# Performance work log

Hardware: AMD Instinct MI355X
Metric: run time of the kernel (lower is better)

Reference implementation:

```python
import jax, jax.numpy as jnp
import numpy as np

B, C, H, W = 32, 256, 32, 32   # batch, channels (inplanes==planes), spatial
E = 8                          # num_experts
EPS = 1e-5                     # BatchNorm eps


def setup_inputs() -> dict:
    key = jax.random.key(0)
    ks = jax.random.split(key, 6)
    s = 0.05
    return {
        "x": jax.random.normal(ks[0], (B, C, H, W), dtype=jnp.float32),
        # router: GAP -> Linear(C, E) -> sigmoid
        "router_w": jax.random.normal(ks[1], (E, C), dtype=jnp.float32) * s,
        "router_b": jnp.zeros((E,), dtype=jnp.float32),
        # expert kernel banks for the two CondConv2d layers (OIHW per expert)
        "w1": jax.random.normal(ks[2], (E, C, C, 3, 3), dtype=jnp.float32) * s,
        "w2": jax.random.normal(ks[3], (E, C, C, 3, 3), dtype=jnp.float32) * s,
        # BatchNorm (eval mode: running stats) params for bn1/bn2
        "g1": jnp.ones((C,), jnp.float32), "b1": jnp.zeros((C,), jnp.float32),
        "m1": jnp.zeros((C,), jnp.float32), "v1": jnp.ones((C,), jnp.float32),
        "g2": jnp.ones((C,), jnp.float32), "b2": jnp.zeros((C,), jnp.float32),
        "m2": jnp.zeros((C,), jnp.float32), "v2": jnp.ones((C,), jnp.float32),
    }


def _bn(x, g, b, m, v):
    # eval-mode BatchNorm over channel dim 1
    scale = (g * jax.lax.rsqrt(v + EPS))[None, :, None, None]
    shift = (b - m * g * jax.lax.rsqrt(v + EPS))[None, :, None, None]
    return x * scale + shift


def _cond_conv(x, w_bank, r):
    # x: [B,C,H,W]; w_bank: [E,O,I,3,3]; r: [B,E]
    # combine expert kernels per sample, then per-sample 3x3 conv (pad=1, stride=1)
    k = jnp.einsum('be,eoihw->boihw', r, w_bank)  # [B,O,I,3,3]

    def one(xb, kb):
        return jax.lax.conv_general_dilated(
            xb[None], kb, window_strides=(1, 1), padding=[(1, 1), (1, 1)],
            dimension_numbers=('NCHW', 'OIHW', 'NCHW'))[0]

    return jax.vmap(one)(x, k)  # [B,O,H,W]


def reference(x, router_w, router_b, w1, w2, g1, b1, m1, v1, g2, b2, m2, v2):
    # BasicRouter: global average pool -> linear -> sigmoid
    r = jax.nn.sigmoid(jnp.mean(x, axis=(2, 3)) @ router_w.T + router_b)  # [B,E]
    # drop_expert is identity in eval mode (training=False)
    out = jax.nn.relu(_bn(_cond_conv(x, w1, r), g1, b1, m1, v1))
    out = _bn(_cond_conv(out, w2, r), g2, b2, m2, v2)
    return jax.nn.relu(out + x)  # identity residual (stride=1, inplanes==planes)
```

## Files before the change

### kernel.cpp

```cpp
#include <hip/hip_runtime.h>

typedef unsigned short ushort_t;
typedef __attribute__((ext_vector_type(8))) __bf16 bf16x8;
typedef __attribute__((ext_vector_type(4))) float f32x4;
typedef __attribute__((ext_vector_type(4))) int i32x4;
typedef __attribute__((ext_vector_type(4))) unsigned short u16x4;

#define BN_EPS 1e-5f
#define EPAD 136

#define BAR()    __builtin_amdgcn_s_barrier()
#define VMCNT0() asm volatile("s_waitcnt vmcnt(0)" ::: "memory")
#define LGKM0()  asm volatile("s_waitcnt lgkmcnt(0)" ::: "memory")

__device__ __forceinline__ ushort_t f2bf(float f) {
    union { float f; unsigned u; } v; v.f = f;
    unsigned r = v.u + 0x7FFFu + ((v.u >> 16) & 1u);
    return (ushort_t)(r >> 16);
}
__device__ __forceinline__ float bf2f(ushort_t h) {
    union { unsigned u; float f; } v; v.u = ((unsigned)h) << 16; return v.f;
}

__device__ __forceinline__ void async_cp16(const ushort_t* g, ushort_t* l) {
    __builtin_amdgcn_global_load_lds(
        (const __attribute__((address_space(1))) unsigned int*)g,
        (__attribute__((address_space(3))) unsigned int*)l, 16, 0, 0);
}

__global__ void transpose_gap_kernel(const float* __restrict__ x, ushort_t* __restrict__ xt,
                                     float* __restrict__ gpart) {
    __shared__ float tile[32][33];
    int b = blockIdx.z, c0 = blockIdx.y * 32, p0 = blockIdx.x * 32;
    int t = threadIdx.x;
    int c = t >> 3, q = t & 7;
    f32x4 v = *(const f32x4*)(x + ((long)b * 256 + c0 + c) * 1024 + p0 + q * 4);
    tile[c][q * 4 + 0] = v[0];
    tile[c][q * 4 + 1] = v[1];
    tile[c][q * 4 + 2] = v[2];
    tile[c][q * 4 + 3] = v[3];
    float ps = v[0] + v[1] + v[2] + v[3];
    ps += __shfl_down(ps, 4, 8);
    ps += __shfl_down(ps, 2, 8);
    ps += __shfl_down(ps, 1, 8);
    if (q == 0) gpart[((long)b * 256 + c0 + c) * 32 + blockIdx.x] = ps;
    __syncthreads();
    int p = t >> 3, coff = (t & 7) * 4;
    u16x4 pk;
    #pragma unroll
    for (int i = 0; i < 4; ++i) pk[i] = f2bf(tile[coff + i][p]);
    *(u16x4*)(xt + ((long)b * 1024 + p0 + p) * 256 + c0 + coff) = pk;
}

__global__ void router_linear_kernel(const float* __restrict__ gpart, const float* __restrict__ rw,
                                     const float* __restrict__ rb, float* __restrict__ r) {
    int be = blockIdx.x;
    int b = be >> 3, e = be & 7;
    int lane = threadIdx.x;
    float s = 0.f;
    #pragma unroll
    for (int i = 0; i < 4; ++i) {
        int c = lane + i * 64;
        const f32x4* gp = (const f32x4*)(gpart + ((long)b * 256 + c) * 32);
        float g = 0.f;
        #pragma unroll
        for (int j = 0; j < 8; ++j) { f32x4 v = gp[j]; g += (v[0] + v[1]) + (v[2] + v[3]); }
        s += g * rw[e * 256 + c];
    }
    #pragma unroll
    for (int off = 32; off; off >>= 1) s += __shfl_down(s, off, 64);
    if (lane == 0) r[be] = 1.f / (1.f + expf(-(s * (1.f / 1024.f) + rb[e])));
}

__global__ __launch_bounds__(256, 2) void combine_kernel(const float* __restrict__ w,
                                                         const float* __restrict__ r,
                                                         ushort_t* __restrict__ ko) {
    __shared__ float wl[9216];
    ushort_t* outb = (ushort_t*)wl;
    const int t = threadIdx.x;
    const int g0 = blockIdx.x * 128;

    #pragma unroll
    for (int it = 0; it < 9; ++it) {
        int lin = it * 256 + t;
        int e = lin / 288, rem = lin - e * 288;
        f32x4 v = *(const f32x4*)(w + (long)e * 589824 + (long)g0 * 9 + rem * 4);
        *(f32x4*)(&wl[lin * 4]) = v;
    }
    __syncthreads();

    const int g = t & 127;
    const int half = t >> 7;
    float wv[8][9];
    #pragma unroll
    for (int e = 0; e < 8; ++e)
        #pragma unroll
        for (int p = 0; p < 9; ++p)
            wv[e][p] = wl[e * 1152 + g * 9 + p];
    __syncthreads();

    #pragma unroll
    for (int hb = 0; hb < 2; ++hb) {
        #pragma unroll
        for (int j = 0; j < 8; ++j) {
            int b16 = half * 8 + j;
            int b = hb * 16 + b16;
            float rv[8];
            #pragma unroll
            for (int e = 0; e < 8; ++e) rv[e] = r[b * 8 + e];
            #pragma unroll
            for (int p = 0; p < 9; ++p) {
                float s = 0.f;
                #pragma unroll
                for (int e = 0; e < 8; ++e) s += rv[e] * wv[e][p];
                outb[(b16 * 9 + p) * 128 + g] = f2bf(s);
            }
        }
        __syncthreads();
        #pragma unroll
        for (int it = 0; it < 9; ++it) {
            int idx = it * 256 + t;
            int row = idx >> 4, off = idx & 15;
            int b16 = row / 9, p = row - b16 * 9;
            i32x4 v = *(i32x4*)(&outb[row * 128 + off * 8]);
            *(i32x4*)(ko + ((long)((hb * 16 + b16) * 9 + p)) * 65536 + g0 + off * 8) = v;
        }
        __syncthreads();
    }
}

template <int MODE>
__global__ __launch_bounds__(256, 2) void gemm_conv(
    const ushort_t* __restrict__ xin,
    const ushort_t* __restrict__ kbank,
    void* __restrict__ outp,
    const float* __restrict__ gam, const float* __restrict__ bet,
    const float* __restrict__ mu, const float* __restrict__ var,
    const ushort_t* __restrict__ residt) {
    __shared__ ushort_t smem[29440];
    ushort_t* ldsB = smem;
    ushort_t* ldsA = smem + 13056;

    const int t = threadIdx.x;
    const int lane = t & 63;
    const int lane15 = lane & 15;
    const int quad = lane >> 4;
    const int wv = t >> 6;
    const int id = blockIdx.x;
    const int q  = id >> 3;
    const int mt = q & 1;
    const int nt = (q >> 1) & 7;
    const int b  = (id & 7) + ((q >> 4) << 3);
    const int h0 = nt * 4;
    const int p0 = nt * 128;
    const int mw0 = (wv >> 1) * 64;
    const int nw0 = (wv & 1) * 64;
    const int wbase = t & ~63;

    f32x4 acc[4][4];
    #pragma unroll
    for (int i = 0; i < 4; ++i)
        #pragma unroll
        for (int j = 0; j < 4; ++j) acc[i][j] = 0.f;

    if (t < 96) {
        int rix = t >> 3, j = t & 7;
        int pi = (rix >> 1) * 34 + (rix & 1) * 33;
        i32x4 z = 0;
        *(i32x4*)(&ldsB[(pi * 8 + j) * 8]) = z;
    }
    if (nt == 0) { i32x4 z = 0; *(i32x4*)(&ldsB[(8 + t) * 8]) = z; }
    if (nt == 7) { i32x4 z = 0; *(i32x4*)(&ldsB[((5 * 34 + 1) * 8 + t) * 8]) = z; }

    const long xbase = (long)b * 1024 * 256;
    const long kbase = (long)b * 9 * 65536;

    auto stageB = [&](int kc) {
        #pragma unroll
        for (int hh = 0; hh < 6; ++hh) {
            int hg = h0 + hh - 1;
            if (hg < 0 || hg >= 32) continue;
            int ww = t >> 3;
            int pi = hh * 34 + 1 + ww;
            int jd = (t & 7) ^ (pi & 7);
            async_cp16(xin + xbase + (long)(hg * 32 + ww) * 256 + kc * 64 + jd * 8,
                       ldsB + ((hh * 34 + 1) * 8 + wbase) * 8);
        }
    };
    auto stageA = [&](int kc, int pos, int buf) {
        const ushort_t* srcA = kbank + kbase + (long)pos * 65536 + (long)mt * 32768 + kc * 64;
        ushort_t* base = ldsA + buf * 8192;
        #pragma unroll
        for (int it = 0; it < 4; ++it) {
            int s = it * 256 + t;
            int row = s >> 3;
            int k8 = (s & 7) ^ (row & 7);
            async_cp16(srcA + (long)row * 256 + k8 * 8, base + (it * 256 + wbase) * 8);
        }
    };

    stageB(0);
    stageA(0, 0, 0);
    __syncthreads();

    int par = 0;
    for (int kc = 0; kc < 4; ++kc) {
        for (int pos = 0; pos < 9; ++pos) {
            const bool last = (kc == 3 && pos == 8);
            VMCNT0();
            BAR();
            if (!last) {
                int nk = kc, np = pos + 1;
                if (np == 9) { np = 0; ++nk; }
                stageA(nk, np, par ^ 1);
            }

            const int dh = pos / 3 - 1, dw = pos % 3 - 1;
            const ushort_t* ab = ldsA + par * 8192;
            bf16x8 af[2][4], bfr[2][4];
            #pragma unroll
            for (int kb = 0; kb < 2; ++kb) {
                int jk = kb * 4 + quad;
                #pragma unroll
                for (int mf = 0; mf < 4; ++mf) {
                    int row = mw0 + mf * 16 + lane15;
                    af[kb][mf] = *(const bf16x8*)(ab + (row * 8 + (jk ^ (row & 7))) * 8);
                }
                #pragma unroll
                for (int nf = 0; nf < 4; ++nf) {
                    int n = nw0 + nf * 16 + lane15;
                    int pi = ((n >> 5) + 1 + dh) * 34 + (n & 31) + 1 + dw;
                    bfr[kb][nf] = *(const bf16x8*)(&ldsB[(pi * 8 + (jk ^ (pi & 7))) * 8]);
                }
            }
            __builtin_amdgcn_s_setprio(1);
            #pragma unroll
            for (int kb = 0; kb < 2; ++kb)
                #pragma unroll
                for (int mf = 0; mf < 4; ++mf)
                    #pragma unroll
                    for (int nf = 0; nf < 4; ++nf)
                        acc[mf][nf] = __builtin_amdgcn_mfma_f32_16x16x32_bf16(af[kb][mf], bfr[kb][nf], acc[mf][nf], 0, 0, 0);
            __builtin_amdgcn_s_setprio(0);

            if (pos == 8 && kc < 3) {
                LGKM0();
                BAR();
                stageB(kc + 1);
            }
            par ^= 1;
        }
    }

    u16x4 rres[4][4];
    if (MODE == 1) {
        #pragma unroll
        for (int mf = 0; mf < 4; ++mf)
            #pragma unroll
            for (int nf = 0; nf < 4; ++nf) {
                int p = p0 + nw0 + nf * 16 + lane15;
                int cb = mt * 128 + mw0 + mf * 16 + quad * 4;
                rres[mf][nf] = *(const u16x4*)(residt + ((long)b * 1024 + p) * 256 + cb);
            }
    }

    float sc[4][4], sh[4][4];
    #pragma unroll
    for (int mf = 0; mf < 4; ++mf)
        #pragma unroll
        for (int i = 0; i < 4; ++i) {
            int c = mt * 128 + mw0 + mf * 16 + quad * 4 + i;
            float s = gam[c] * rsqrtf(var[c] + BN_EPS);
            sc[mf][i] = s;
            sh[mf][i] = bet[c] - mu[c] * s;
        }

    if (MODE == 0) {
        __syncthreads();
        ushort_t* ldsE = smem;
        #pragma unroll
        for (int mf = 0; mf < 4; ++mf)
            #pragma unroll
            for (int nf = 0; nf < 4; ++nf) {
                int pl = nw0 + nf * 16 + lane15;
                int cb = mw0 + mf * 16 + quad * 4;
                u16x4 pk;
                #pragma unroll
                for (int i = 0; i < 4; ++i) {
                    float v = acc[mf][nf][i] * sc[mf][i] + sh[mf][i];
                    pk[i] = f2bf(fmaxf(v, 0.f));
                }
                *(u16x4*)(&ldsE[pl * EPAD + cb]) = pk;
            }
        __syncthreads();
        ushort_t* op = (ushort_t*)outp;
        #pragma unroll
        for (int it = 0; it < 8; ++it) {
            int s = t + it * 256;
            int row = s >> 4, l16 = s & 15;
            i32x4 v = *(i32x4*)(&ldsE[row * EPAD + l16 * 8]);
            *(i32x4*)(op + ((long)b * 1024 + p0 + row) * 256 + mt * 128 + l16 * 8) = v;
        }
    } else {
        float* op = (float*)outp;
        #pragma unroll
        for (int mf = 0; mf < 4; ++mf)
            #pragma unroll
            for (int nf = 0; nf < 4; ++nf) {
                int p = p0 + nw0 + nf * 16 + lane15;
                #pragma unroll
                for (int i = 0; i < 4; ++i) {
                    int c = mt * 128 + mw0 + mf * 16 + quad * 4 + i;
                    float v = acc[mf][nf][i] * sc[mf][i] + sh[mf][i] + bf2f(rres[mf][nf][i]);
                    op[((long)b * 256 + c) * 1024 + p] = fmaxf(v, 0.f);
                }
            }
    }
}

extern "C" void kernel_launch(void* const* d_in, const int* in_sizes, int n_in,
                              void* d_out, int out_size, void* d_ws, size_t ws_size,
                              hipStream_t stream) {
    const float* x  = (const float*)d_in[0];
    const float* rw = (const float*)d_in[1];
    const float* rb = (const float*)d_in[2];
    const float* w1 = (const float*)d_in[3];
    const float* w2 = (const float*)d_in[4];
    const float* g1 = (const float*)d_in[5];
    const float* b1 = (const float*)d_in[6];
    const float* m1 = (const float*)d_in[7];
    const float* v1 = (const float*)d_in[8];
    const float* g2 = (const float*)d_in[9];
    const float* b2 = (const float*)d_in[10];
    const float* m2 = (const float*)d_in[11];
    const float* v2 = (const float*)d_in[12];

    const size_t GP_OFF  = 4096;
    const size_t XT_OFF  = GP_OFF + (size_t)1048576;
    const size_t O1_OFF  = XT_OFF + (size_t)16777216;
    const size_t KB_OFF  = O1_OFF + (size_t)16777216;
    const size_t NEED    = KB_OFF + (size_t)32 * 9 * 65536 * 2;
    if (ws_size < NEED) return;

    char* ws = (char*)d_ws;
    float* r       = (float*)ws;
    float* gpart   = (float*)(ws + GP_OFF);
    ushort_t* xt   = (ushort_t*)(ws + XT_OFF);
    ushort_t* o1   = (ushort_t*)(ws + O1_OFF);
    ushort_t* kbuf = (ushort_t*)(ws + KB_OFF);

    transpose_gap_kernel<<<dim3(32, 8, 32), 256, 0, stream>>>(x, xt, gpart);
    router_linear_kernel<<<256, 64, 0, stream>>>(gpart, rw, rb, r);
    combine_kernel<<<dim3(512), 256, 0, stream>>>(w1, r, kbuf);
    gemm_conv<0><<<512, 256, 0, stream>>>(xt, kbuf, (void*)o1, g1, b1, m1, v1, nullptr);
    combine_kernel<<<dim3(512), 256, 0, stream>>>(w2, r, kbuf);
    gemm_conv<1><<<512, 256, 0, stream>>>(o1, kbuf, d_out, g2, b2, m2, v2, xt);
}
```

Measured before the change: 227.6 us.

## Co-schedule second kernel combine with first conv GEMM in one launch

Splits combine and GEMM into device bodies and adds a fused kernel whose first 512 blocks build the second layer's per-sample kernels while the remaining blocks run the first conv GEMM. A second kernel buffer lets the two run at once without a hazard, which removes one launch and lets the memory-bound combine overlap the compute-bound GEMM. It needs extra workspace and falls back to the old sequence when the workspace is too small. The merged kernel may also raise register or LDS pressure for the combine blocks.

```diff
diff --git a/kernel.cpp b/kernel.cpp
--- a/kernel.cpp
+++ b/kernel.cpp
@@ -72,13 +72,11 @@
     if (lane == 0) r[be] = 1.f / (1.f + expf(-(s * (1.f / 1024.f) + rb[e])));
 }
 
-__global__ __launch_bounds__(256, 2) void combine_kernel(const float* __restrict__ w,
-                                                         const float* __restrict__ r,
-                                                         ushort_t* __restrict__ ko) {
-    __shared__ float wl[9216];
+__device__ __forceinline__ void combine_body(int bid, float* wl, const float* __restrict__ w,
+                                             const float* __restrict__ r, ushort_t* __restrict__ ko) {
     ushort_t* outb = (ushort_t*)wl;
     const int t = threadIdx.x;
-    const int g0 = blockIdx.x * 128;
+    const int g0 = bid * 128;
 
     #pragma unroll
     for (int it = 0; it < 9; ++it) {
@@ -130,14 +128,11 @@
 }
 
 template <int MODE>
-__global__ __launch_bounds__(256, 2) void gemm_conv(
-    const ushort_t* __restrict__ xin,
-    const ushort_t* __restrict__ kbank,
-    void* __restrict__ outp,
+__device__ __forceinline__ void gemm_body(int id, ushort_t* smem,
+    const ushort_t* __restrict__ xin, const ushort_t* __restrict__ kbank, void* __restrict__ outp,
     const float* __restrict__ gam, const float* __restrict__ bet,
     const float* __restrict__ mu, const float* __restrict__ var,
     const ushort_t* __restrict__ residt) {
-    __shared__ ushort_t smem[29440];
     ushort_t* ldsB = smem;
     ushort_t* ldsA = smem + 13056;
 
@@ -146,7 +141,6 @@
     const int lane15 = lane & 15;
     const int quad = lane >> 4;
     const int wv = t >> 6;
-    const int id = blockIdx.x;
     const int q  = id >> 3;
     const int mt = q & 1;
     const int nt = (q >> 1) & 7;
@@ -315,6 +309,36 @@
                     op[((long)b * 256 + c) * 1024 + p] = fmaxf(v, 0.f);
                 }
             }
+    }
+}
+
+__global__ __launch_bounds__(256, 2) void combine_kernel(const float* __restrict__ w,
+                                                         const float* __restrict__ r,
+                                                         ushort_t* __restrict__ ko) {
+    __shared__ __align__(16) float wl[9216];
+    combine_body(blockIdx.x, wl, w, r, ko);
+}
+
+template <int MODE>
+__global__ __launch_bounds__(256, 2) void gemm_conv(
+    const ushort_t* __restrict__ xin, const ushort_t* __restrict__ kbank, void* __restrict__ outp,
+    const float* __restrict__ gam, const float* __restrict__ bet,
+    const float* __restrict__ mu, const float* __restrict__ var,
+    const ushort_t* __restrict__ residt) {
+    __shared__ __align__(16) ushort_t smem[29440];
+    gemm_body<MODE>(blockIdx.x, smem, xin, kbank, outp, gam, bet, mu, var, residt);
+}
+
+__global__ __launch_bounds__(256, 2) void gemm1_combine2_kernel(
+    const ushort_t* __restrict__ xt, const ushort_t* __restrict__ kb1, ushort_t* __restrict__ o1,
+    const float* __restrict__ g1, const float* __restrict__ b1,
+    const float* __restrict__ m1, const float* __restrict__ v1,
+    const float* __restrict__ w2, const float* __restrict__ r, ushort_t* __restrict__ kb2) {
+    __shared__ __align__(16) ushort_t smem[29440];
+    if (blockIdx.x < 512) {
+        combine_body(blockIdx.x, (float*)smem, w2, r, kb2);
+    } else {
+        gemm_body<0>(blockIdx.x - 512, smem, xt, kb1, (void*)o1, g1, b1, m1, v1, nullptr);
     }
 }
 
@@ -335,24 +359,34 @@
     const float* m2 = (const float*)d_in[11];
     const float* v2 = (const float*)d_in[12];
 
+    const size_t KBSZ    = (size_t)32 * 9 * 65536 * 2;
     const size_t GP_OFF  = 4096;
     const size_t XT_OFF  = GP_OFF + (size_t)1048576;
     const size_t O1_OFF  = XT_OFF + (size_t)16777216;
     const size_t KB_OFF  = O1_OFF + (size_t)16777216;
-    const size_t NEED    = KB_OFF + (size_t)32 * 9 * 65536 * 2;
-    if (ws_size < NEED) return;
+    const size_t KB2_OFF = KB_OFF + KBSZ;
+    const size_t NEED_S  = KB_OFF + KBSZ;
+    const size_t NEED_F  = KB2_OFF + KBSZ;
+    if (ws_size < NEED_S) return;
+    const bool fused = (ws_size >= NEED_F);
 
     char* ws = (char*)d_ws;
     float* r       = (float*)ws;
     float* gpart   = (float*)(ws + GP_OFF);
     ushort_t* xt   = (ushort_t*)(ws + XT_OFF);
     ushort_t* o1   = (ushort_t*)(ws + O1_OFF);
-    ushort_t* kbuf = (ushort_t*)(ws + KB_OFF);
+    ushort_t* kb1  = (ushort_t*)(ws + KB_OFF);
+    ushort_t* kb2  = (ushort_t*)(ws + KB2_OFF);
 
     transpose_gap_kernel<<<dim3(32, 8, 32), 256, 0, stream>>>(x, xt, gpart);
     router_linear_kernel<<<256, 64, 0, stream>>>(gpart, rw, rb, r);
-    combine_kernel<<<dim3(512), 256, 0, stream>>>(w1, r, kbuf);
-    gemm_conv<0><<<512, 256, 0, stream>>>(xt, kbuf, (void*)o1, g1, b1, m1, v1, nullptr);
-    combine_kernel<<<dim3(512), 256, 0, stream>>>(w2, r, kbuf);
-    gemm_conv<1><<<512, 256, 0, stream>>>(o1, kbuf, d_out, g2, b2, m2, v2, xt);
-}
+    combine_kernel<<<dim3(512), 256, 0, stream>>>(w1, r, kb1);
+    if (fused) {
+        gemm1_combine2_kernel<<<1024, 256, 0, stream>>>(xt, kb1, o1, g1, b1, m1, v1, w2, r, kb2);
+        gemm_conv<1><<<512, 256, 0, stream>>>(o1, kb2, d_out, g2, b2, m2, v2, xt);
+    } else {
+        gemm_conv<0><<<512, 256, 0, stream>>>(xt, kb1, (void*)o1, g1, b1, m1, v1, nullptr);
+        combine_kernel<<<dim3(512), 256, 0, stream>>>(w2, r, kb1);
+        gemm_conv<1><<<512, 256, 0, stream>>>(o1, kb1, d_out, g2, b2, m2, v2, xt);
+    }
+}
```

After: 228.7 us. Within noise of the previous version (+0.5%).
